# Optimization experiments

Measured on AMD Instinct MI355X. Metric: run time of the kernel, lower is better.

## Reference

```python
import jax, jax.numpy as jnp
import numpy as np
import math

N_EXPERTS = 64
CAPACITY_FACTOR = 1.25


def setup_inputs() -> dict:
    key = jax.random.key(0)
    k1, k2 = jax.random.split(key)
    N, TOP_K = 131072, 2
    dispatch_weights = jax.random.uniform(k1, (N, TOP_K), dtype=jnp.float32)
    expert_indices = jax.random.randint(k2, (N, TOP_K), 0, N_EXPERTS, dtype=jnp.int64)
    return {"dispatch_weights": dispatch_weights, "expert_indices": expert_indices, "n_tokens": N}


def reference(dispatch_weights, expert_indices, n_tokens):
    N, top_k = dispatch_weights.shape
    capacity = max(1, int(math.ceil(CAPACITY_FACTOR * n_tokens * top_k / N_EXPERTS)))

    # Original loops slot-major: for slot in range(top_k): for tok in range(N).
    # Flatten in that same (slot, token) order so ranks match the serial counter.
    flat_e = expert_indices.T.reshape(-1)  # (top_k*N,) int
    onehot = jax.nn.one_hot(flat_e, N_EXPERTS, dtype=jnp.int32)  # (top_k*N, E)
    # inclusive cumulative per-expert count; rank within expert = inclusive - 1
    incl = jnp.cumsum(onehot, axis=0)
    rank = jnp.take_along_axis(incl, flat_e[:, None].astype(jnp.int32), axis=1)[:, 0] - 1
    keep_flat = rank < capacity  # (top_k*N,)
    keep = keep_flat.reshape(top_k, N).T  # back to (N, top_k)

    weights_capped = jnp.where(keep, dispatch_weights, jnp.zeros((), dtype=dispatch_weights.dtype))
    overflow_mask = weights_capped.sum(axis=-1) == 0.0
    return weights_capped, expert_indices, overflow_mask
```

## Files before the change

kernel.cpp:

```cpp
#include <hip/hip_runtime.h>
#include <math.h>

#define N_EXPERTS 64
#define BLOCK 256

__global__ __launch_bounds__(BLOCK) void ExpertCapacityBuffer_80444737454353_kernel(
    const float* __restrict__ weights,
    const int*   __restrict__ experts,
    float*       __restrict__ out,
    int*         __restrict__ counts,
    int N, int capacity)
{
    __shared__ int local_cnt[N_EXPERTS];
    __shared__ int base[N_EXPERTS];

    const int tid = threadIdx.x;
    if (tid < N_EXPERTS) local_cnt[tid] = 0;
    __syncthreads();

    const int t = blockIdx.x * BLOCK + tid;
    float2 wv = make_float2(0.f, 0.f);
    int2   ev = make_int2(0, 0);
    int r0 = 0, r1 = 0;
    const bool active = (t < N);
    if (active) {
        wv = ((const float2*)weights)[t];
        ev = ((const int2*)experts)[t];
        r0 = atomicAdd(&local_cnt[ev.x], 1);
        r1 = atomicAdd(&local_cnt[ev.y], 1);
    }
    __syncthreads();

    if (tid < N_EXPERTS) {
        int c = local_cnt[tid];
        base[tid] = (c > 0) ? atomicAdd(&counts[tid], c) : 0;
    }
    __syncthreads();

    if (active) {
        const int rank0 = base[ev.x] + r0;
        const int rank1 = base[ev.y] + r1;
        const float wc0 = (rank0 < capacity) ? wv.x : 0.0f;
        const float wc1 = (rank1 < capacity) ? wv.y : 0.0f;

        ((float2*)out)[t] = make_float2(wc0, wc1);
        ((float2*)(out + 2 * (size_t)N))[t] =
            make_float2((float)ev.x, (float)ev.y);
        out[4 * (size_t)N + t] = ((wc0 + wc1) == 0.0f) ? 1.0f : 0.0f;
    }
}

extern "C" void kernel_launch(void* const* d_in, const int* in_sizes, int n_in,
                              void* d_out, int out_size, void* d_ws, size_t ws_size,
                              hipStream_t stream) {
    const float* weights = (const float*)d_in[0];
    const int*   experts = (const int*)d_in[1];
    float*       out     = (float*)d_out;

    const int N = in_sizes[0] / 2;
    int capacity = (int)ceil(1.25 * (double)N * 2.0 / (double)N_EXPERTS);
    if (capacity < 1) capacity = 1;

    int* counts = (int*)d_ws;
    hipMemsetAsync(d_ws, 0, N_EXPERTS * sizeof(int), stream);

    const int blocks = (N + BLOCK - 1) / BLOCK;
    hipLaunchKernelGGL(ExpertCapacityBuffer_80444737454353_kernel,
                       dim3(blocks), dim3(BLOCK), 0, stream,
                       weights, experts, out, counts, N, capacity);
}
```

Measured before the change: 68.63 us.

## Replace global atomic expert counters with per-block histogram and prefix pass

The single kernel, which claimed each block's rank base with global atomicAdd on 64 counters after a memset, is split into two kernels. A histogram kernel writes per-block expert counts. The main kernel then sums the histograms of all earlier blocks, with 4 partitions of 64 threads, to get each block's base. This removes the memset and global atomic contention and makes ranks deterministic in block order. In exchange it adds a second launch and a prefix read that grows with the block index, roughly quadratic L2 traffic overall.

```diff
diff --git a/kernel.cpp b/kernel.cpp
--- a/kernel.cpp
+++ b/kernel.cpp
@@ -4,40 +4,67 @@
 #define N_EXPERTS 64
 #define BLOCK 256
 
-__global__ __launch_bounds__(BLOCK) void ExpertCapacityBuffer_80444737454353_kernel(
+__global__ __launch_bounds__(BLOCK) void ExpertCapacityBuffer_hist_kernel(
+    const int* __restrict__ experts,
+    int*       __restrict__ hist,
+    int N)
+{
+    __shared__ int local_cnt[N_EXPERTS];
+    const int tid = threadIdx.x;
+    if (tid < N_EXPERTS) local_cnt[tid] = 0;
+    __syncthreads();
+
+    const int t = blockIdx.x * BLOCK + tid;
+    if (t < N) {
+        const int2 ev = ((const int2*)experts)[t];
+        atomicAdd(&local_cnt[ev.x], 1);
+        atomicAdd(&local_cnt[ev.y], 1);
+    }
+    __syncthreads();
+
+    if (tid < N_EXPERTS) hist[blockIdx.x * N_EXPERTS + tid] = local_cnt[tid];
+}
+
+__global__ __launch_bounds__(BLOCK) void ExpertCapacityBuffer_main_kernel(
     const float* __restrict__ weights,
     const int*   __restrict__ experts,
     float*       __restrict__ out,
-    int*         __restrict__ counts,
+    const int*   __restrict__ hist,
     int N, int capacity)
 {
     __shared__ int local_cnt[N_EXPERTS];
     __shared__ int base[N_EXPERTS];
+    __shared__ int partial[BLOCK];
 
     const int tid = threadIdx.x;
     if (tid < N_EXPERTS) local_cnt[tid] = 0;
     __syncthreads();
 
     const int t = blockIdx.x * BLOCK + tid;
+    const bool act = (t < N);
     float2 wv = make_float2(0.f, 0.f);
     int2   ev = make_int2(0, 0);
     int r0 = 0, r1 = 0;
-    const bool active = (t < N);
-    if (active) {
+    if (act) {
         wv = ((const float2*)weights)[t];
         ev = ((const int2*)experts)[t];
         r0 = atomicAdd(&local_cnt[ev.x], 1);
         r1 = atomicAdd(&local_cnt[ev.y], 1);
     }
+
+    const int e = tid & (N_EXPERTS - 1);
+    const int part = tid >> 6;
+    int s = 0;
+    for (int b = part; b < (int)blockIdx.x; b += 4)
+        s += hist[b * N_EXPERTS + e];
+    partial[tid] = s;
     __syncthreads();
 
-    if (tid < N_EXPERTS) {
-        int c = local_cnt[tid];
-        base[tid] = (c > 0) ? atomicAdd(&counts[tid], c) : 0;
-    }
+    if (tid < N_EXPERTS)
+        base[tid] = partial[tid] + partial[tid + 64] + partial[tid + 128] + partial[tid + 192];
     __syncthreads();
 
-    if (active) {
+    if (act) {
         const int rank0 = base[ev.x] + r0;
         const int rank1 = base[ev.y] + r1;
         const float wc0 = (rank0 < capacity) ? wv.x : 0.0f;
@@ -61,11 +88,13 @@
     int capacity = (int)ceil(1.25 * (double)N * 2.0 / (double)N_EXPERTS);
     if (capacity < 1) capacity = 1;
 
-    int* counts = (int*)d_ws;
-    hipMemsetAsync(d_ws, 0, N_EXPERTS * sizeof(int), stream);
+    int* hist = (int*)d_ws;
+    const int blocks = (N + BLOCK - 1) / BLOCK;
 
-    const int blocks = (N + BLOCK - 1) / BLOCK;
-    hipLaunchKernelGGL(ExpertCapacityBuffer_80444737454353_kernel,
+    hipLaunchKernelGGL(ExpertCapacityBuffer_hist_kernel,
                        dim3(blocks), dim3(BLOCK), 0, stream,
-                       weights, experts, out, counts, N, capacity);
+                       experts, hist, N);
+    hipLaunchKernelGGL(ExpertCapacityBuffer_main_kernel,
+                       dim3(blocks), dim3(BLOCK), 0, stream,
+                       weights, experts, out, hist, N, capacity);
 }
```

Measured after the change: 76.47 us. 1.11x slower.
